# Kernel tuning notes

Measured on AMD Instinct MI355X. Metric: run time of the kernel, lower is better.

## Reference

```python
import jax, jax.numpy as jnp
import numpy as np

B, S, D, H = 4, 2048, 1024, 16
DH = D // H


def setup_inputs() -> dict:
    key = jax.random.key(0)
    ks = jax.random.split(key, 12)
    s = 0.02
    inp = {
        "q": jax.random.normal(ks[0], (B, S, D), jnp.float32),
        "k": jax.random.normal(ks[1], (B, S, D), jnp.float32),
        "v": jax.random.normal(ks[2], (B, S, D), jnp.float32),
        # causal mask, broadcastable over batch and heads (mask==0 -> -1e9)
        "mask": jnp.tril(jnp.ones((S, S), jnp.int32))[None, None, :, :],
        "wq": jax.random.normal(ks[3], (D, D), jnp.float32) * s,
        "bq": jnp.zeros((D,), jnp.float32),
        "wk": jax.random.normal(ks[4], (D, D), jnp.float32) * s,
        "bk": jnp.zeros((D,), jnp.float32),
        "wv": jax.random.normal(ks[5], (D, D), jnp.float32) * s,
        "bv": jnp.zeros((D,), jnp.float32),
        "wo": jax.random.normal(ks[6], (D, D), jnp.float32) * s,
        "bo": jnp.zeros((D,), jnp.float32),
    }
    return inp


def reference(q, k, v, mask, wq, bq, wk, bk, wv, bv, wo, bo):
    # linear projections (torch Linear: x @ W^T + b)
    qh = (q @ wq.T + bq).reshape(B, S, H, DH).transpose(0, 2, 1, 3)  # [B,H,S,DH]
    kh = (k @ wk.T + bk).reshape(B, S, H, DH).transpose(0, 2, 1, 3)
    vh = (v @ wv.T + bv).reshape(B, S, H, DH).transpose(0, 2, 1, 3)
    scale = 1.0 / jnp.sqrt(jnp.float32(DH))
    score = jnp.einsum("bhqd,bhkd->bhqk", qh, kh) * scale  # [B,H,S,S]
    score = jnp.where(mask == 0, jnp.float32(-1e9), score)
    attn = jax.nn.softmax(score, axis=-1)
    ctx = jnp.einsum("bhqk,bhkd->bhqd", attn, vh)  # [B,H,S,DH]
    ctx = ctx.transpose(0, 2, 1, 3).reshape(B, S, D)
    return ctx @ wo.T + bo
```

## Files before the change

kernel.cpp:

```cpp
#include <hip/hip_runtime.h>
#include <hip/hip_bf16.h>

#define NB 4
#define NS 2048
#define ND 1024
#define NH 16
#define NDH 64
#define E_ 8388608
#define W_ 1048576

typedef __attribute__((ext_vector_type(8))) __bf16 bf16x8;
typedef __attribute__((ext_vector_type(4))) float f32x4;
typedef __attribute__((ext_vector_type(2))) unsigned int u32x2;
typedef unsigned short us16;
typedef unsigned int u32;

__device__ __forceinline__ unsigned short f2bf(float f) {
  union { float f; unsigned u; } v; v.f = f;
  unsigned r = v.u + 0x7FFFu + ((v.u >> 16) & 1u);
  return (unsigned short)(r >> 16);
}

typedef const __attribute__((address_space(1))) unsigned int* gas_t;
typedef __attribute__((address_space(3))) unsigned int* las_t;
__device__ __forceinline__ void gl2lds16(const void* g, void* l) {
  __builtin_amdgcn_global_load_lds((gas_t)g, (las_t)l, 16, 0, 0);
}

__global__ __launch_bounds__(256) void conv_bf16(
    const float* __restrict__ q, const float* __restrict__ k, const float* __restrict__ v,
    const float* __restrict__ wq, const float* __restrict__ wk, const float* __restrict__ wv,
    const float* __restrict__ wo,
    us16* __restrict__ qb, us16* __restrict__ kb, us16* __restrict__ vb,
    us16* __restrict__ wqb, us16* __restrict__ wkb, us16* __restrict__ wvb,
    us16* __restrict__ wob)
{
  int b = blockIdx.x;
  int seg, off;
  if (b < 24576) { seg = b >> 13; off = b & 8191; }
  else { b -= 24576; seg = 3 + (b >> 10); off = b & 1023; }
  const float* s; us16* d;
  switch (seg) {
    case 0: s = q;  d = qb;  break;
    case 1: s = k;  d = kb;  break;
    case 2: s = v;  d = vb;  break;
    case 3: s = wq; d = wqb; break;
    case 4: s = wk; d = wkb; break;
    case 5: s = wv; d = wvb; break;
    default: s = wo; d = wob; break;
  }
  size_t idx = ((size_t)off * 256 + threadIdx.x) * 4;
  float4 f = *(const float4*)(s + idx);
  ushort4 u;
  u.x = f2bf(f.x); u.y = f2bf(f.y); u.z = f2bf(f.z); u.w = f2bf(f.w);
  *(ushort4*)(d + idx) = u;
}

__global__ __launch_bounds__(256, 3) void gemm_proj(
    const us16* __restrict__ A, const us16* __restrict__ Wt,
    const float* __restrict__ bias, us16* __restrict__ out, float scale, int mode)
{
  __shared__ us16 As[128][64];
  __shared__ us16 Bs[128][64];
  const int tid = threadIdx.x;
  const int lane = tid & 63;
  const int w = tid >> 6;
  const int l15 = lane & 15, quad = lane >> 4;
  const int sw = l15 & 7;
  const int rowBase = blockIdx.x * 128, colBase = blockIdx.y * 128;
  const int srow = w * 32 + (lane >> 3);
  const int cu = (lane & 7) ^ ((lane >> 3) & 7);
  const us16* ga = A  + (size_t)(rowBase + srow) * ND + cu * 8;
  const us16* gb = Wt + (size_t)(colBase + srow) * ND + cu * 8;
  const int wr = (w >> 1) * 64, wc = (w & 1) * 64;

  f32x4 acc[4][4] = {};
  for (int kt = 0; kt < ND; kt += 64) {
    __syncthreads();
    #pragma unroll
    for (int c = 0; c < 4; ++c) {
      gl2lds16(ga + kt + c * 8 * ND, &As[w * 32 + c * 8][0]);
      gl2lds16(gb + kt + c * 8 * ND, &Bs[w * 32 + c * 8][0]);
    }
    __syncthreads();
    #pragma unroll
    for (int ks = 0; ks < 2; ++ks) {
      bf16x8 af[4], bfr[4];
      #pragma unroll
      for (int i = 0; i < 4; ++i)
        af[i]  = *(const bf16x8*)&As[wr + i * 16 + l15][((ks * 4 + quad) ^ sw) * 8];
      #pragma unroll
      for (int j = 0; j < 4; ++j)
        bfr[j] = *(const bf16x8*)&Bs[wc + j * 16 + l15][((ks * 4 + quad) ^ sw) * 8];
      #pragma unroll
      for (int i = 0; i < 4; ++i)
        #pragma unroll
        for (int j = 0; j < 4; ++j)
          acc[i][j] = __builtin_amdgcn_mfma_f32_16x16x32_bf16(af[i], bfr[j], acc[i][j], 0, 0, 0);
    }
  }

  if (mode < 2) {
    #pragma unroll
    for (int i = 0; i < 4; ++i) {
      #pragma unroll
      for (int j = 0; j < 4; ++j) {
        int colg = colBase + wc + j * 16 + l15;
        float bval = bias[colg];
        int h_ = colg >> 6, d_ = colg & 63;
        #pragma unroll
        for (int r = 0; r < 4; ++r) {
          int rowg = rowBase + wr + i * 16 + quad * 4 + r;
          int b_ = rowg >> 11, s_ = rowg & (NS - 1);
          out[(((size_t)(b_ * NH + h_) * NS) + s_) * NDH + d_] = f2bf((acc[i][j][r] + bval) * scale);
        }
      }
    }
  } else {
    #pragma unroll
    for (int i = 0; i < 4; ++i) {
      #pragma unroll
      for (int j = 0; j < 4; ++j) {
        int colg = colBase + wc + j * 16 + l15;
        float bval = bias[colg];
        int h_ = colg >> 6, d_ = colg & 63;
        int rowg0 = rowBase + wr + i * 16 + quad * 4;
        int b_ = rowg0 >> 11, s0 = rowg0 & (NS - 1);
        ushort4 vv;
        vv.x = f2bf(acc[i][j][0] + bval);
        vv.y = f2bf(acc[i][j][1] + bval);
        vv.z = f2bf(acc[i][j][2] + bval);
        vv.w = f2bf(acc[i][j][3] + bval);
        *(ushort4*)(out + ((size_t)(b_ * NH + h_) * NDH + d_) * NS + s0) = vv;
      }
    }
  }
}

__global__ __launch_bounds__(256, 3) void attn(
    const us16* __restrict__ Qh, const us16* __restrict__ Kh,
    const us16* __restrict__ Vht, us16* __restrict__ ctx)
{
  __shared__ us16 Ks[64][64];
  __shared__ us16 Vts[64][64];
  __shared__ us16 Ps[4][32][136];
  us16* Qs = &Ps[0][0][0];

  const int bh = blockIdx.y, b_ = bh >> 4, h_ = bh & 15;
  const int qb0 = ((int)gridDim.x - 1 - (int)blockIdx.x) * 128;
  const int tid = threadIdx.x, lane = tid & 63, w = tid >> 6;
  const int l15 = lane & 15, quad = lane >> 4;
  const int sw = l15 & 7;
  const int lr8 = lane >> 3;
  const int cu = (lane & 7) ^ (lr8 & 7);

  {
    const us16* gq = Qh + ((size_t)bh * NS + qb0 + w * 32 + lr8) * NDH + (lane & 7) * 8;
    #pragma unroll
    for (int u = 0; u < 4; ++u)
      gl2lds16(gq + u * 8 * NDH, Qs + (w * 32 + u * 8) * 64);
  }
  __syncthreads();
  bf16x8 bq[2][2];
  #pragma unroll
  for (int ntl = 0; ntl < 2; ++ntl)
    #pragma unroll
    for (int c = 0; c < 2; ++c)
      bq[ntl][c] = *(const bf16x8*)(Qs + (w * 32 + ntl * 16 + l15) * 64 + c * 32 + quad * 8);

  f32x4 o[2][4] = {};
  float lsum[2] = {0.f, 0.f};
  const int qw = qb0 + w * 32;
  const int qg0 = qw + l15, qg1 = qw + 16 + l15;

  const us16* gk = Kh  + ((size_t)bh * NS + w * 16 + lr8) * NDH + cu * 8;
  const us16* gv = Vht + ((size_t)bh * NDH + w * 16 + lr8) * NS + cu * 8;

  const int nt = qb0 / 64 + 2;
  for (int it = 0; it < nt; ++it) {
    const int kb = it * 64;
    __syncthreads();
    gl2lds16(gk + (size_t)kb * NDH,           &Ks[w * 16][0]);
    gl2lds16(gk + (size_t)(kb + 8) * NDH,     &Ks[w * 16 + 8][0]);
    gl2lds16(gv + kb,                         &Vts[w * 16][0]);
    gl2lds16(gv + kb + 8 * NS,                &Vts[w * 16 + 8][0]);
    __syncthreads();

    if (kb <= qw + 31) {
      const bool full = (kb + 63 <= qw);
      #pragma unroll
      for (int mt = 0; mt < 4; ++mt) {
        bf16x8 ak0 = *(const bf16x8*)&Ks[mt * 16 + l15][(quad ^ sw) * 8];
        bf16x8 ak1 = *(const bf16x8*)&Ks[mt * 16 + l15][((4 + quad) ^ sw) * 8];
        #pragma unroll
        for (int ntl = 0; ntl < 2; ++ntl) {
          f32x4 s = {};
          s = __builtin_amdgcn_mfma_f32_16x16x32_bf16(ak0, bq[ntl][0], s, 0, 0, 0);
          s = __builtin_amdgcn_mfma_f32_16x16x32_bf16(ak1, bq[ntl][1], s, 0, 0, 0);
          u32 u[4];
          if (full) {
            #pragma unroll
            for (int r = 0; r < 4; ++r) {
              float p = __builtin_amdgcn_exp2f(s[r]);
              lsum[ntl] += p;
              u[r] = __float_as_uint(p);
            }
          } else {
            const int keyb = kb + mt * 16 + quad * 4;
            const int qg = ntl ? qg1 : qg0;
            #pragma unroll
            for (int r = 0; r < 4; ++r) {
              float p = (keyb + r <= qg) ? __builtin_amdgcn_exp2f(s[r]) : 0.f;
              lsum[ntl] += p;
              u[r] = __float_as_uint(p);
            }
          }
          u32 lo = (u[0] >> 16) | (u[1] & 0xffff0000u);
          u32 hi = (u[2] >> 16) | (u[3] & 0xffff0000u);
          *(u32x2*)&Ps[w][ntl * 16 + l15][mt * 16 + quad * 4] = (u32x2){lo, hi};
        }
      }
      #pragma unroll
      for (int c = 0; c < 2; ++c) {
        bf16x8 bv[4];
        #pragma unroll
        for (int n = 0; n < 4; ++n)
          bv[n] = *(const bf16x8*)&Vts[n * 16 + l15][((c * 4 + quad) ^ sw) * 8];
        #pragma unroll
        for (int ntl = 0; ntl < 2; ++ntl) {
          bf16x8 ap = *(const bf16x8*)&Ps[w][ntl * 16 + l15][c * 32 + quad * 8];
          #pragma unroll
          for (int n = 0; n < 4; ++n)
            o[ntl][n] = __builtin_amdgcn_mfma_f32_16x16x32_bf16(ap, bv[n], o[ntl][n], 0, 0, 0);
        }
      }
    }
  }

  #pragma unroll
  for (int ntl = 0; ntl < 2; ++ntl) {
    lsum[ntl] += __shfl_xor(lsum[ntl], 16, 64);
    lsum[ntl] += __shfl_xor(lsum[ntl], 32, 64);
  }
  #pragma unroll
  for (int ntl = 0; ntl < 2; ++ntl) {
    #pragma unroll
    for (int r = 0; r < 4; ++r) {
      float lrow = __shfl(lsum[ntl], quad * 4 + r, 64);
      float inv = __builtin_amdgcn_rcpf(lrow);
      int qg = qb0 + w * 32 + ntl * 16 + quad * 4 + r;
      us16* dst = ctx + ((size_t)b_ * NS + qg) * ND + h_ * NDH;
      #pragma unroll
      for (int n = 0; n < 4; ++n)
        dst[n * 16 + l15] = f2bf(o[ntl][n][r] * inv);
    }
  }
}

__global__ __launch_bounds__(256, 3) void gemm_out(
    const us16* __restrict__ A, const us16* __restrict__ Wt,
    const float* __restrict__ bias, float* __restrict__ out)
{
  __shared__ us16 As[128][64];
  __shared__ us16 Bs[128][64];
  const int tid = threadIdx.x;
  const int lane = tid & 63;
  const int w = tid >> 6;
  const int l15 = lane & 15, quad = lane >> 4;
  const int sw = l15 & 7;
  const int rowBase = blockIdx.x * 128, colBase = blockIdx.y * 128;
  const int srow = w * 32 + (lane >> 3);
  const int cu = (lane & 7) ^ ((lane >> 3) & 7);
  const us16* ga = A  + (size_t)(rowBase + srow) * ND + cu * 8;
  const us16* gb = Wt + (size_t)(colBase + srow) * ND + cu * 8;
  const int wr = (w >> 1) * 64, wc = (w & 1) * 64;

  f32x4 acc[4][4] = {};
  for (int kt = 0; kt < ND; kt += 64) {
    __syncthreads();
    #pragma unroll
    for (int c = 0; c < 4; ++c) {
      gl2lds16(ga + kt + c * 8 * ND, &As[w * 32 + c * 8][0]);
      gl2lds16(gb + kt + c * 8 * ND, &Bs[w * 32 + c * 8][0]);
    }
    __syncthreads();
    #pragma unroll
    for (int ks = 0; ks < 2; ++ks) {
      bf16x8 af[4], bfr[4];
      #pragma unroll
      for (int i = 0; i < 4; ++i)
        af[i]  = *(const bf16x8*)&As[wr + i * 16 + l15][((ks * 4 + quad) ^ sw) * 8];
      #pragma unroll
      for (int j = 0; j < 4; ++j)
        bfr[j] = *(const bf16x8*)&Bs[wc + j * 16 + l15][((ks * 4 + quad) ^ sw) * 8];
      #pragma unroll
      for (int i = 0; i < 4; ++i)
        #pragma unroll
        for (int j = 0; j < 4; ++j)
          acc[i][j] = __builtin_amdgcn_mfma_f32_16x16x32_bf16(af[i], bfr[j], acc[i][j], 0, 0, 0);
    }
  }

  #pragma unroll
  for (int i = 0; i < 4; ++i) {
    #pragma unroll
    for (int j = 0; j < 4; ++j) {
      int colg = colBase + wc + j * 16 + l15;
      float bval = bias[colg];
      #pragma unroll
      for (int r = 0; r < 4; ++r) {
        int rowg = rowBase + wr + i * 16 + quad * 4 + r;
        out[(size_t)rowg * ND + colg] = acc[i][j][r] + bval;
      }
    }
  }
}

extern "C" void kernel_launch(void* const* d_in, const int* in_sizes, int n_in,
                              void* d_out, int out_size, void* d_ws, size_t ws_size,
                              hipStream_t stream) {
  const float* q  = (const float*)d_in[0];
  const float* k  = (const float*)d_in[1];
  const float* v  = (const float*)d_in[2];
  const float* wq = (const float*)d_in[4];
  const float* bq = (const float*)d_in[5];
  const float* wk = (const float*)d_in[6];
  const float* bk = (const float*)d_in[7];
  const float* wv = (const float*)d_in[8];
  const float* bv = (const float*)d_in[9];
  const float* wo = (const float*)d_in[10];
  const float* bo = (const float*)d_in[11];

  us16* ws = (us16*)d_ws;
  us16* qb  = ws;
  us16* kb  = ws + (size_t)E_;
  us16* vb  = ws + (size_t)2 * E_;
  us16* wqb = ws + (size_t)3 * E_;
  us16* wkb = wqb + W_;
  us16* wvb = wkb + W_;
  us16* wob = wvb + W_;
  us16* Kh  = qb;
  us16* ctx = vb;
  us16* Vht = (us16*)d_out;
  us16* Qh  = (us16*)d_out + (size_t)E_;

  const float qscale = 0.125f * 1.44269504088896340736f;

  conv_bf16<<<28672, 256, 0, stream>>>(q, k, v, wq, wk, wv, wo,
                                       qb, kb, vb, wqb, wkb, wvb, wob);
  gemm_proj<<<dim3(64, 8), 256, 0, stream>>>(qb, wqb, bq, Qh, qscale, 0);
  gemm_proj<<<dim3(64, 8), 256, 0, stream>>>(vb, wvb, bv, Vht, 1.0f, 2);
  gemm_proj<<<dim3(64, 8), 256, 0, stream>>>(kb, wkb, bk, Kh, 1.0f, 1);
  attn<<<dim3(NS / 128, NB * NH), 256, 0, stream>>>(Qh, Kh, Vht, ctx);
  gemm_out<<<dim3(64, 8), 256, 0, stream>>>(ctx, wob, bo, (float*)d_out);
}
```

Measured before the change: 351.3 us.

## Restructure attention with paired causal tiles, double-buffered K/V, MFMA row sums

The attention kernel now gives each block two query tiles, pr and 15-pr, so causal work is balanced across a 512-block 1D grid. K/V tiles are double-buffered so the next tile's loads overlap compute, and the P buffer is shrunk with a swizzle. Row sums come from an MFMA against a ones vector instead of scalar accumulation plus shuffles. Q and K projections now write in row-major [B,S,D] layout that attention reads with strided access, and the Q and V projections are merged into one launch via blockIdx.z. Occupancy is raised to 4 blocks per SM, and the row sums now use the bf16-rounded probabilities.

```diff
diff --git a/kernel.cpp b/kernel.cpp
--- a/kernel.cpp
+++ b/kernel.cpp
@@ -56,10 +56,17 @@
   *(ushort4*)(d + idx) = u;
 }
 
-__global__ __launch_bounds__(256, 3) void gemm_proj(
-    const us16* __restrict__ A, const us16* __restrict__ Wt,
-    const float* __restrict__ bias, us16* __restrict__ out, float scale, int mode)
+__global__ __launch_bounds__(256, 3) void gemm_qv(
+    const us16* __restrict__ A0, const us16* __restrict__ A1,
+    const us16* __restrict__ W0, const us16* __restrict__ W1,
+    const float* __restrict__ bias0, const float* __restrict__ bias1,
+    us16* __restrict__ out0, us16* __restrict__ out1, float scale)
 {
+  const int z = blockIdx.z;
+  const us16* A  = z ? A1 : A0;
+  const us16* Wt = z ? W1 : W0;
+  const float* bias = z ? bias1 : bias0;
+
   __shared__ us16 As[128][64];
   __shared__ us16 Bs[128][64];
   const int tid = threadIdx.x;
@@ -100,19 +107,17 @@
     }
   }
 
-  if (mode < 2) {
+  if (z == 0) {
     #pragma unroll
     for (int i = 0; i < 4; ++i) {
       #pragma unroll
       for (int j = 0; j < 4; ++j) {
         int colg = colBase + wc + j * 16 + l15;
         float bval = bias[colg];
-        int h_ = colg >> 6, d_ = colg & 63;
         #pragma unroll
         for (int r = 0; r < 4; ++r) {
           int rowg = rowBase + wr + i * 16 + quad * 4 + r;
-          int b_ = rowg >> 11, s_ = rowg & (NS - 1);
-          out[(((size_t)(b_ * NH + h_) * NS) + s_) * NDH + d_] = f2bf((acc[i][j][r] + bval) * scale);
+          out0[(size_t)rowg * ND + colg] = f2bf((acc[i][j][r] + bval) * scale);
         }
       }
     }
@@ -131,128 +136,144 @@
         vv.y = f2bf(acc[i][j][1] + bval);
         vv.z = f2bf(acc[i][j][2] + bval);
         vv.w = f2bf(acc[i][j][3] + bval);
-        *(ushort4*)(out + ((size_t)(b_ * NH + h_) * NDH + d_) * NS + s0) = vv;
-      }
-    }
-  }
-}
-
-__global__ __launch_bounds__(256, 3) void attn(
+        *(ushort4*)(out1 + ((size_t)(b_ * NH + h_) * NDH + d_) * NS + s0) = vv;
+      }
+    }
+  }
+}
+
+__global__ __launch_bounds__(256, 4) void attn(
     const us16* __restrict__ Qh, const us16* __restrict__ Kh,
     const us16* __restrict__ Vht, us16* __restrict__ ctx)
 {
-  __shared__ us16 Ks[64][64];
-  __shared__ us16 Vts[64][64];
-  __shared__ us16 Ps[4][32][136];
-  us16* Qs = &Ps[0][0][0];
-
-  const int bh = blockIdx.y, b_ = bh >> 4, h_ = bh & 15;
-  const int qb0 = ((int)gridDim.x - 1 - (int)blockIdx.x) * 128;
+  __shared__ us16 Ks[2][64][64];
+  __shared__ us16 Vts[2][64][64];
+  __shared__ us16 Ps[4][32][32];
+  us16* Qsta = &Vts[0][0][0];
+
+  const int bh = blockIdx.x >> 3;
+  const int pr = blockIdx.x & 7;
+  const int b_ = bh >> 4, h_ = bh & 15;
   const int tid = threadIdx.x, lane = tid & 63, w = tid >> 6;
   const int l15 = lane & 15, quad = lane >> 4;
   const int sw = l15 & 7;
   const int lr8 = lane >> 3;
   const int cu = (lane & 7) ^ (lr8 & 7);
 
-  {
-    const us16* gq = Qh + ((size_t)bh * NS + qb0 + w * 32 + lr8) * NDH + (lane & 7) * 8;
-    #pragma unroll
-    for (int u = 0; u < 4; ++u)
-      gl2lds16(gq + u * 8 * NDH, Qs + (w * 32 + u * 8) * 64);
-  }
-  __syncthreads();
-  bf16x8 bq[2][2];
+  bf16x8 ones;
   #pragma unroll
-  for (int ntl = 0; ntl < 2; ++ntl)
-    #pragma unroll
-    for (int c = 0; c < 2; ++c)
-      bq[ntl][c] = *(const bf16x8*)(Qs + (w * 32 + ntl * 16 + l15) * 64 + c * 32 + quad * 8);
-
-  f32x4 o[2][4] = {};
-  float lsum[2] = {0.f, 0.f};
-  const int qw = qb0 + w * 32;
-  const int qg0 = qw + l15, qg1 = qw + 16 + l15;
-
-  const us16* gk = Kh  + ((size_t)bh * NS + w * 16 + lr8) * NDH + cu * 8;
-  const us16* gv = Vht + ((size_t)bh * NDH + w * 16 + lr8) * NS + cu * 8;
-
-  const int nt = qb0 / 64 + 2;
-  for (int it = 0; it < nt; ++it) {
-    const int kb = it * 64;
-    __syncthreads();
-    gl2lds16(gk + (size_t)kb * NDH,           &Ks[w * 16][0]);
-    gl2lds16(gk + (size_t)(kb + 8) * NDH,     &Ks[w * 16 + 8][0]);
-    gl2lds16(gv + kb,                         &Vts[w * 16][0]);
-    gl2lds16(gv + kb + 8 * NS,                &Vts[w * 16 + 8][0]);
-    __syncthreads();
-
-    if (kb <= qw + 31) {
-      const bool full = (kb + 63 <= qw);
-      #pragma unroll
-      for (int mt = 0; mt < 4; ++mt) {
-        bf16x8 ak0 = *(const bf16x8*)&Ks[mt * 16 + l15][(quad ^ sw) * 8];
-        bf16x8 ak1 = *(const bf16x8*)&Ks[mt * 16 + l15][((4 + quad) ^ sw) * 8];
-        #pragma unroll
-        for (int ntl = 0; ntl < 2; ++ntl) {
-          f32x4 s = {};
-          s = __builtin_amdgcn_mfma_f32_16x16x32_bf16(ak0, bq[ntl][0], s, 0, 0, 0);
-          s = __builtin_amdgcn_mfma_f32_16x16x32_bf16(ak1, bq[ntl][1], s, 0, 0, 0);
-          u32 u[4];
-          if (full) {
+  for (int i = 0; i < 8; ++i) ones[i] = (__bf16)1.0f;
+
+  const us16* gkbase = Kh  + ((size_t)b_ * NS + w * 16 + lr8) * ND + h_ * NDH + cu * 8;
+  const us16* gvbase = Vht + ((size_t)bh * NDH + w * 16 + lr8) * NS + cu * 8;
+
+  for (int pass = 0; pass < 2; ++pass) {
+    const int tq = pass ? (15 - pr) : pr;
+    const int qb0 = tq * 128;
+    const int nt = tq * 2 + 2;
+    const int qw = qb0 + w * 32;
+
+    __syncthreads();
+    {
+      const us16* gq = Qh + ((size_t)b_ * NS + qb0 + w * 32 + lr8) * ND + h_ * NDH + cu * 8;
+      #pragma unroll
+      for (int u = 0; u < 4; ++u)
+        gl2lds16(gq + (size_t)u * 8 * ND, Qsta + (w * 32 + u * 8) * 64);
+    }
+    __syncthreads();
+    bf16x8 bq[2][2];
+    #pragma unroll
+    for (int ntl = 0; ntl < 2; ++ntl)
+      #pragma unroll
+      for (int c = 0; c < 2; ++c)
+        bq[ntl][c] = *(const bf16x8*)(Qsta + (w * 32 + ntl * 16 + l15) * 64 +
+                                      (((c * 4 + quad) ^ sw) * 8));
+    __syncthreads();
+
+    gl2lds16(gkbase,            &Ks[0][w * 16][0]);
+    gl2lds16(gkbase + 8 * ND,   &Ks[0][w * 16 + 8][0]);
+    gl2lds16(gvbase,            &Vts[0][w * 16][0]);
+    gl2lds16(gvbase + 8 * NS,   &Vts[0][w * 16 + 8][0]);
+
+    f32x4 o[2][4] = {};
+    f32x4 o_l[2] = {};
+
+    for (int it = 0; it < nt; ++it) {
+      const int kb = it * 64;
+      const int cur = it & 1;
+      __syncthreads();
+      if (it + 1 < nt) {
+        const int nxt = cur ^ 1;
+        gl2lds16(gkbase + (size_t)(kb + 64) * ND,          &Ks[nxt][w * 16][0]);
+        gl2lds16(gkbase + (size_t)(kb + 72) * ND,          &Ks[nxt][w * 16 + 8][0]);
+        gl2lds16(gvbase + kb + 64,                         &Vts[nxt][w * 16][0]);
+        gl2lds16(gvbase + kb + 64 + 8 * NS,                &Vts[nxt][w * 16 + 8][0]);
+      }
+      if (kb <= qw + 31) {
+        const bool full = (kb + 63 <= qw);
+        #pragma unroll
+        for (int h2 = 0; h2 < 2; ++h2) {
+          f32x4 s[2][2];
+          #pragma unroll
+          for (int mt = 0; mt < 2; ++mt) {
+            bf16x8 ak0 = *(const bf16x8*)&Ks[cur][h2 * 32 + mt * 16 + l15][(quad ^ sw) * 8];
+            bf16x8 ak1 = *(const bf16x8*)&Ks[cur][h2 * 32 + mt * 16 + l15][((4 + quad) ^ sw) * 8];
             #pragma unroll
-            for (int r = 0; r < 4; ++r) {
-              float p = __builtin_amdgcn_exp2f(s[r]);
-              lsum[ntl] += p;
-              u[r] = __float_as_uint(p);
-            }
-          } else {
-            const int keyb = kb + mt * 16 + quad * 4;
-            const int qg = ntl ? qg1 : qg0;
-            #pragma unroll
-            for (int r = 0; r < 4; ++r) {
-              float p = (keyb + r <= qg) ? __builtin_amdgcn_exp2f(s[r]) : 0.f;
-              lsum[ntl] += p;
-              u[r] = __float_as_uint(p);
+            for (int ntl = 0; ntl < 2; ++ntl) {
+              f32x4 t = {};
+              t = __builtin_amdgcn_mfma_f32_16x16x32_bf16(ak0, bq[ntl][0], t, 0, 0, 0);
+              t = __builtin_amdgcn_mfma_f32_16x16x32_bf16(ak1, bq[ntl][1], t, 0, 0, 0);
+              s[mt][ntl] = t;
             }
           }
-          u32 lo = (u[0] >> 16) | (u[1] & 0xffff0000u);
-          u32 hi = (u[2] >> 16) | (u[3] & 0xffff0000u);
-          *(u32x2*)&Ps[w][ntl * 16 + l15][mt * 16 + quad * 4] = (u32x2){lo, hi};
+          #pragma unroll
+          for (int mt = 0; mt < 2; ++mt)
+            #pragma unroll
+            for (int ntl = 0; ntl < 2; ++ntl) {
+              u32 u[4];
+              if (full) {
+                #pragma unroll
+                for (int r = 0; r < 4; ++r)
+                  u[r] = __float_as_uint(__builtin_amdgcn_exp2f(s[mt][ntl][r]));
+              } else {
+                const int keyb = kb + h2 * 32 + mt * 16 + quad * 4;
+                const int qg = qw + ntl * 16 + l15;
+                #pragma unroll
+                for (int r = 0; r < 4; ++r) {
+                  float p = (keyb + r <= qg) ? __builtin_amdgcn_exp2f(s[mt][ntl][r]) : 0.f;
+                  u[r] = __float_as_uint(p);
+                }
+              }
+              u32 lo = (u[0] >> 16) | (u[1] & 0xffff0000u);
+              u32 hi = (u[2] >> 16) | (u[3] & 0xffff0000u);
+              int uswz = (mt * 2 + (quad >> 1)) ^ (l15 & 3);
+              *(u32x2*)&Ps[w][ntl * 16 + l15][uswz * 8 + (quad & 1) * 4] = (u32x2){lo, hi};
+            }
+          #pragma unroll
+          for (int ntl = 0; ntl < 2; ++ntl) {
+            bf16x8 ap = *(const bf16x8*)&Ps[w][ntl * 16 + l15][(quad ^ (l15 & 3)) * 8];
+            o_l[ntl] = __builtin_amdgcn_mfma_f32_16x16x32_bf16(ap, ones, o_l[ntl], 0, 0, 0);
+            #pragma unroll
+            for (int n = 0; n < 4; ++n) {
+              bf16x8 bv = *(const bf16x8*)&Vts[cur][n * 16 + l15][((h2 * 4 + quad) ^ sw) * 8];
+              o[ntl][n] = __builtin_amdgcn_mfma_f32_16x16x32_bf16(ap, bv, o[ntl][n], 0, 0, 0);
+            }
+          }
         }
       }
-      #pragma unroll
-      for (int c = 0; c < 2; ++c) {
-        bf16x8 bv[4];
+    }
+
+    #pragma unroll
+    for (int ntl = 0; ntl < 2; ++ntl) {
+      #pragma unroll
+      for (int r = 0; r < 4; ++r) {
+        float inv = __builtin_amdgcn_rcpf(o_l[ntl][r]);
+        int qg = qb0 + w * 32 + ntl * 16 + quad * 4 + r;
+        us16* dst = ctx + ((size_t)b_ * NS + qg) * ND + h_ * NDH;
         #pragma unroll
         for (int n = 0; n < 4; ++n)
-          bv[n] = *(const bf16x8*)&Vts[n * 16 + l15][((c * 4 + quad) ^ sw) * 8];
-        #pragma unroll
-        for (int ntl = 0; ntl < 2; ++ntl) {
-          bf16x8 ap = *(const bf16x8*)&Ps[w][ntl * 16 + l15][c * 32 + quad * 8];
-          #pragma unroll
-          for (int n = 0; n < 4; ++n)
-            o[ntl][n] = __builtin_amdgcn_mfma_f32_16x16x32_bf16(ap, bv[n], o[ntl][n], 0, 0, 0);
-        }
-      }
-    }
-  }
-
-  #pragma unroll
-  for (int ntl = 0; ntl < 2; ++ntl) {
-    lsum[ntl] += __shfl_xor(lsum[ntl], 16, 64);
-    lsum[ntl] += __shfl_xor(lsum[ntl], 32, 64);
-  }
-  #pragma unroll
-  for (int ntl = 0; ntl < 2; ++ntl) {
-    #pragma unroll
-    for (int r = 0; r < 4; ++r) {
-      float lrow = __shfl(lsum[ntl], quad * 4 + r, 64);
-      float inv = __builtin_amdgcn_rcpf(lrow);
-      int qg = qb0 + w * 32 + ntl * 16 + quad * 4 + r;
-      us16* dst = ctx + ((size_t)b_ * NS + qg) * ND + h_ * NDH;
-      #pragma unroll
-      for (int n = 0; n < 4; ++n)
-        dst[n * 16 + l15] = f2bf(o[ntl][n][r] * inv);
+          dst[n * 16 + l15] = f2bf(o[ntl][n][r] * inv);
+      }
     }
   }
 }
@@ -323,13 +344,13 @@
   const float* k  = (const float*)d_in[1];
   const float* v  = (const float*)d_in[2];
   const float* wq = (const float*)d_in[4];
-  const float* bq = (const float*)d_in[5];
+  const float* bq_ = (const float*)d_in[5];
   const float* wk = (const float*)d_in[6];
-  const float* bk = (const float*)d_in[7];
+  const float* bk_ = (const float*)d_in[7];
   const float* wv = (const float*)d_in[8];
-  const float* bv = (const float*)d_in[9];
+  const float* bv_ = (const float*)d_in[9];
   const float* wo = (const float*)d_in[10];
-  const float* bo = (const float*)d_in[11];
+  const float* bo_ = (const float*)d_in[11];
 
   us16* ws = (us16*)d_ws;
   us16* qb  = ws;
@@ -348,9 +369,10 @@
 
   conv_bf16<<<28672, 256, 0, stream>>>(q, k, v, wq, wk, wv, wo,
                                        qb, kb, vb, wqb, wkb, wvb, wob);
-  gemm_proj<<<dim3(64, 8), 256, 0, stream>>>(qb, wqb, bq, Qh, qscale, 0);
-  gemm_proj<<<dim3(64, 8), 256, 0, stream>>>(vb, wvb, bv, Vht, 1.0f, 2);
-  gemm_proj<<<dim3(64, 8), 256, 0, stream>>>(kb, wkb, bk, Kh, 1.0f, 1);
-  attn<<<dim3(NS / 128, NB * NH), 256, 0, stream>>>(Qh, Kh, Vht, ctx);
-  gemm_out<<<dim3(64, 8), 256, 0, stream>>>(ctx, wob, bo, (float*)d_out);
-}
+  gemm_qv<<<dim3(64, 8, 2), 256, 0, stream>>>(qb, vb, wqb, wvb, bq_, bv_,
+                                              Qh, Vht, qscale);
+  gemm_qv<<<dim3(64, 8, 1), 256, 0, stream>>>(kb, kb, wkb, wkb, bk_, bk_,
+                                              Kh, Kh, 1.0f);
+  attn<<<512, 256, 0, stream>>>(Qh, Kh, Vht, ctx);
+  gemm_out<<<dim3(64, 8), 256, 0, stream>>>(ctx, wob, bo_, (float*)d_out);
+}
```

Result: faster. 319.9 us (-8.9%).
